# Kernel tuning notes

Hardware: AMD Instinct MI355X
Metric: run time of the kernel (lower is better)

Reference implementation:

```python
import jax, jax.numpy as jnp
import numpy as np
from jax import lax

B, N, M = 2, 16384, 4096
C1, C2 = 128, 256
H1, H2 = 256, 128  # mlp = [C1+C2, 256, 128]


def setup_inputs() -> dict:
    key = jax.random.key(0)
    ks = jax.random.split(key, 8)
    return {
        "unknown": jax.random.normal(ks[0], (B, N, 3), jnp.float32),
        "known": jax.random.normal(ks[1], (B, M, 3), jnp.float32),
        "unknow_feats": jax.random.normal(ks[2], (B, C1, N), jnp.float32),
        "known_feats": jax.random.normal(ks[3], (B, C2, M), jnp.float32),
        "W1": jax.random.normal(ks[4], (H1, C1 + C2), jnp.float32) * 0.05,
        "b1": jnp.zeros((H1,), jnp.float32),
        "W2": jax.random.normal(ks[5], (H2, H1), jnp.float32) * 0.05,
        "b2": jnp.zeros((H2,), jnp.float32),
    }


def reference(unknown, known, unknow_feats, known_feats, W1, b1, W2, b2):
    # Pairwise squared distances (B, n, m) via ||a||^2 + ||b||^2 - 2 a.b
    d2 = (
        jnp.sum(unknown * unknown, -1)[:, :, None]
        + jnp.sum(known * known, -1)[:, None, :]
        - 2.0 * jnp.einsum("bnd,bmd->bnm", unknown, known)
    )
    # 3 nearest neighbors
    neg_d2, idx = lax.top_k(-d2, 3)  # (B, n, 3)
    dist = jnp.sqrt(jnp.maximum(-neg_d2, 0.0))  # pointops returns sqrt distances
    dist_recip = 1.0 / (dist + 1e-8)
    weight = dist_recip / jnp.sum(dist_recip, axis=2, keepdims=True)  # (B, n, 3)
    # Gather neighbor features (B, C2, n, 3) and inverse-distance weighted sum
    gathered = jax.vmap(lambda f, i: f[:, i])(known_feats, idx)
    interpolated = jnp.sum(gathered * weight[:, None, :, :], axis=-1)  # (B, C2, n)
    new_features = jnp.concatenate([interpolated, unknow_feats], axis=1)  # (B, C1+C2, n)
    # Shared MLP (1x1 convs, bn=False -> conv bias + ReLU)
    h = jax.nn.relu(jnp.einsum("oc,bcn->bon", W1, new_features) + b1[None, :, None])
    out = jax.nn.relu(jnp.einsum("oc,bcn->bon", W2, h) + b2[None, :, None])
    return out  # (B, mlp[-1], n)
```

## Files before the change

### kernel.cpp

```cpp
#include <hip/hip_runtime.h>
#include <hip/hip_bf16.h>

#define BB 2
#define NN 16384
#define MM 4096
#define C1 128
#define C2 256
#define CIN 384
#define H1 256
#define H2 128
#define XROW 392
#define HROW 264

typedef __attribute__((ext_vector_type(8))) short bf16x8;
typedef __attribute__((ext_vector_type(4))) float f32x4;
typedef __attribute__((ext_vector_type(2))) float f32x2;

__device__ __forceinline__ short f32_to_bf16(float x) {
    unsigned u = __float_as_uint(x);
    u += 0x7fffu + ((u >> 16) & 1u);
    return (short)(u >> 16);
}
__device__ __forceinline__ float bf16_to_f32(unsigned short u) {
    union { unsigned u; float f; } c; c.u = ((unsigned)u) << 16; return c.f;
}
__device__ __forceinline__ unsigned pack_bf16x2(float a, float b) {
    __hip_bfloat162 h = __float22bfloat162_rn(make_float2(a, b));
    union { __hip_bfloat162 h; unsigned u; } cv;
    cv.h = h;
    return cv.u;
}
__device__ __forceinline__ f32x2 score2l(f32x2 ax2, f32x2 ay2, f32x2 az2,
                                         f32x2 kx, f32x2 ky, f32x2 kz, f32x2 kn) {
    f32x2 t = __builtin_elementwise_fma(ay2, ky, kn);
    t = __builtin_elementwise_fma(ax2, kx, t);
    t = __builtin_elementwise_fma(az2, kz, t);
    return t;
}

__global__ __launch_bounds__(256) void prep_kernel(
    const float* __restrict__ KF, unsigned short* __restrict__ KT16,
    const float* __restrict__ W1, const float* __restrict__ W2,
    short* __restrict__ W1b, short* __restrict__ W2b,
    const float* __restrict__ known, float* __restrict__ kpk8)
{
    const int bx  = blockIdx.x;
    const int tid = threadIdx.x;
    if (bx < 2048) {
        __shared__ float tl[32][33];
        const int b  = bx >> 10;
        const int c0 = ((bx >> 7) & 7) * 32;
        const int m0 = (bx & 127) * 32;
        const int tx = tid & 31;
        const int ty = tid >> 5;
        #pragma unroll
        for (int r = 0; r < 4; ++r) {
            int c = ty + r * 8;
            tl[c][tx] = KF[((size_t)b * C2 + c0 + c) * MM + m0 + tx];
        }
        __syncthreads();
        #pragma unroll
        for (int r = 0; r < 4; ++r) {
            int m = ty + r * 8;
            KT16[((size_t)b * MM + m0 + m) * C2 + c0 + tx] =
                (unsigned short)f32_to_bf16(tl[tx][m]);
        }
    } else if (bx < 2432) {
        int i = (bx - 2048) * 256 + tid;
        if (i < H1 * CIN) W1b[i] = f32_to_bf16(W1[i]);
        if (i < H2 * H1)  W2b[i] = f32_to_bf16(W2[i]);
    } else {
        int i = (bx - 2432) * 256 + tid;
        if (i < BB * MM) {
            float x = known[3 * i + 0], y = known[3 * i + 1], z = known[3 * i + 2];
            float n = fmaf(x, x, fmaf(y, y, z * z));
            int g = i >> 1, j = i & 1;
            float* base = kpk8 + (size_t)g * 8;
            base[0 + j] = x; base[2 + j] = y; base[4 + j] = z; base[6 + j] = n;
        }
    }
}

__global__ __launch_bounds__(1024, 8) void fused_knn_mlp_kernel(
    const float* __restrict__ unknown,
    const float* __restrict__ kpk8,
    const float* __restrict__ unknow_feats,
    const unsigned short* __restrict__ KT16,
    const short* __restrict__ W1b, const float* __restrict__ b1,
    const short* __restrict__ W2b, const float* __restrict__ b2,
    float* __restrict__ out)
{
    __shared__ __align__(16) float cand[16384];
    __shared__ __align__(16) float red[3072];
    __shared__ float vf[64];
    __shared__ int   cnt[64];
    __shared__ int   IsL[64 * 3];
    __shared__ float WsL[64 * 3];

    const int bx    = blockIdx.x;
    const int tid   = threadIdx.x;
    const int lane  = tid & 63;
    const int w     = __builtin_amdgcn_readfirstlane(tid >> 6);
    const int b     = bx >> 8;
    const int qbase = (bx & 255) * 64;
    const int n     = qbase + lane;

    if (tid < 64) cnt[tid] = 0;

    {
        const float* kb = kpk8 + (size_t)b * 16384;
        #pragma unroll
        for (int c = 0; c < 4; ++c) {
            const int i = c * 4096 + tid * 4;
            *(f32x4*)&cand[i] = *(const f32x4*)(kb + i);
        }
    }

    {
        const float ux = unknown[((size_t)b * NN + n) * 3 + 0];
        const float uy = unknown[((size_t)b * NN + n) * 3 + 1];
        const float uz = unknown[((size_t)b * NN + n) * 3 + 2];
        const f32x2 ax2 = {-2.f * ux, -2.f * ux};
        const f32x2 ay2 = {-2.f * uy, -2.f * uy};
        const f32x2 az2 = {-2.f * uz, -2.f * uz};
        const float un = fmaf(ux, ux, fmaf(uy, uy, uz * uz));

        const int gbase = w * 128;
        const float* kw = cand + w * 1024;
        __syncthreads();

        float va0 = 3e38f, va1 = 3e38f, va2 = 3e38f;
        float vb0 = 3e38f, vb1 = 3e38f, vb2 = 3e38f;
        #pragma unroll 4
        for (int g = 0; g < 128; ++g) {
            const f32x4 P = *(const f32x4*)(kw + g * 8);
            const f32x4 Q = *(const f32x4*)(kw + g * 8 + 4);
            const f32x2 kx = {P.x, P.y};
            const f32x2 ky = {P.z, P.w};
            const f32x2 kz = {Q.x, Q.y};
            const f32x2 kn = {Q.z, Q.w};
            const f32x2 sc2 = score2l(ax2, ay2, az2, kx, ky, kz, kn);
            float sa = sc2.x;
            va2 = __builtin_amdgcn_fmed3f(va1, sa, va2);
            va1 = __builtin_amdgcn_fmed3f(va0, sa, va1);
            va0 = fminf(sa, va0);
            float sb = sc2.y;
            vb2 = __builtin_amdgcn_fmed3f(vb1, sb, vb2);
            vb1 = __builtin_amdgcn_fmed3f(vb0, sb, vb1);
            vb0 = fminf(sb, vb0);
        }
        {
            float bv[3] = {vb0, vb1, vb2};
            #pragma unroll
            for (int k = 0; k < 3; ++k) {
                float d = bv[k];
                va2 = __builtin_amdgcn_fmed3f(va1, d, va2);
                va1 = __builtin_amdgcn_fmed3f(va0, d, va1);
                va0 = fminf(d, va0);
            }
        }
        red[(w * 64 + lane) * 3 + 0] = va0;
        red[(w * 64 + lane) * 3 + 1] = va1;
        red[(w * 64 + lane) * 3 + 2] = va2;
        __syncthreads();

        if (tid < 64) {
            float r0 = 3e38f, r1 = 3e38f, r2 = 3e38f;
            #pragma unroll
            for (int ww = 0; ww < 16; ++ww) {
                #pragma unroll
                for (int k = 0; k < 3; ++k) {
                    float d = red[(ww * 64 + tid) * 3 + k];
                    r2 = __builtin_amdgcn_fmed3f(r1, d, r2);
                    r1 = __builtin_amdgcn_fmed3f(r0, d, r1);
                    r0 = fminf(d, r0);
                }
            }
            vf[tid] = r2;
        }
        __syncthreads();

        float* mscp = red;
        int*   midp = (int*)red + 512;
        const float v2f = vf[lane];
        #pragma unroll 4
        for (int g = 0; g < 128; ++g) {
            const f32x4 P = *(const f32x4*)(kw + g * 8);
            const f32x4 Q = *(const f32x4*)(kw + g * 8 + 4);
            const f32x2 kx = {P.x, P.y};
            const f32x2 ky = {P.z, P.w};
            const f32x2 kz = {Q.x, Q.y};
            const f32x2 kn = {Q.z, Q.w};
            const f32x2 sc2 = score2l(ax2, ay2, az2, kx, ky, kz, kn);
            if (fminf(sc2.x, sc2.y) <= v2f) {
                if (sc2.x <= v2f) {
                    int c = atomicAdd(&cnt[lane], 1);
                    if (c < 8) { mscp[lane * 8 + c] = sc2.x; midp[lane * 8 + c] = (gbase + g) * 2; }
                }
                if (sc2.y <= v2f) {
                    int c = atomicAdd(&cnt[lane], 1);
                    if (c < 8) { mscp[lane * 8 + c] = sc2.y; midp[lane * 8 + c] = (gbase + g) * 2 + 1; }
                }
            }
        }
        __syncthreads();

        if (tid < 64) {
            const int c = cnt[tid] < 8 ? cnt[tid] : 8;
            float r0 = 3e38f, r1 = 3e38f, r2 = 3e38f;
            int   q0 = 0x7FFFFFFF, q1 = 0x7FFFFFFF, q2 = 0x7FFFFFFF;
            #pragma unroll
            for (int k = 0; k < 8; ++k) {
                float d = (k < c) ? mscp[tid * 8 + k] : 3e38f;
                int   j = (k < c) ? midp[tid * 8 + k] : 0x7FFFFFFF;
                const bool lt0 = (d < r0) || (d == r0 && j < q0);
                const bool lt1 = (d < r1) || (d == r1 && j < q1);
                const bool lt2 = (d < r2) || (d == r2 && j < q2);
                float nr2 = lt1 ? r1 : (lt2 ? d : r2);
                int   nq2 = lt1 ? q1 : (lt2 ? j : q2);
                float nr1 = lt0 ? r0 : (lt1 ? d : r1);
                int   nq1 = lt0 ? q0 : (lt1 ? j : q1);
                float nr0 = lt0 ? d : r0;
                int   nq0 = lt0 ? j : q0;
                r0 = nr0; r1 = nr1; r2 = nr2; q0 = nq0; q1 = nq1; q2 = nq2;
            }
            float d0 = sqrtf(fmaxf(r0 + un, 0.f));
            float d1 = sqrtf(fmaxf(r1 + un, 0.f));
            float d2 = sqrtf(fmaxf(r2 + un, 0.f));
            float i0 = 1.f / (d0 + 1e-8f);
            float i1 = 1.f / (d1 + 1e-8f);
            float i2 = 1.f / (d2 + 1e-8f);
            float s  = i0 + i1 + i2;
            IsL[tid * 3 + 0] = q0; IsL[tid * 3 + 1] = q1; IsL[tid * 3 + 2] = q2;
            WsL[tid * 3 + 0] = i0 / s; WsL[tid * 3 + 1] = i1 / s; WsL[tid * 3 + 2] = i2 / s;
        }
    }
    __syncthreads();

    const unsigned short* KTb = KT16 + (size_t)b * MM * C2;
    short* XH_s = (short*)cand;
    short* Hs_s = (short*)cand + 32 * XROW;
    const int lr = lane & 15;
    const int lq = lane >> 4;
    const int c4 = lane << 2;

    for (int tile = 0; tile < 2; ++tile) {
        const int pbase = tile * 32;

        {
            ushort4 g[2][3];
            #pragma unroll
            for (int j = 0; j < 2; ++j) {
                const int pi = (pbase + 2 * w + j) * 3;
                g[j][0] = *(const ushort4*)(KTb + (size_t)IsL[pi + 0] * C2 + c4);
                g[j][1] = *(const ushort4*)(KTb + (size_t)IsL[pi + 1] * C2 + c4);
                g[j][2] = *(const ushort4*)(KTb + (size_t)IsL[pi + 2] * C2 + c4);
            }
            #pragma unroll
            for (int j = 0; j < 2; ++j) {
                const int pl = 2 * w + j;
                const int pi = (pbase + pl) * 3;
                const float w0 = WsL[pi + 0], w1 = WsL[pi + 1], w2 = WsL[pi + 2];
                float vx = fmaf(w0, bf16_to_f32(g[j][0].x), fmaf(w1, bf16_to_f32(g[j][1].x), w2 * bf16_to_f32(g[j][2].x)));
                float vy = fmaf(w0, bf16_to_f32(g[j][0].y), fmaf(w1, bf16_to_f32(g[j][1].y), w2 * bf16_to_f32(g[j][2].y)));
                float vz = fmaf(w0, bf16_to_f32(g[j][0].z), fmaf(w1, bf16_to_f32(g[j][1].z), w2 * bf16_to_f32(g[j][2].z)));
                float vw = fmaf(w0, bf16_to_f32(g[j][0].w), fmaf(w1, bf16_to_f32(g[j][1].w), w2 * bf16_to_f32(g[j][2].w)));
                uint2 pk;
                pk.x = pack_bf16x2(vx, vy);
                pk.y = pack_bf16x2(vz, vw);
                *(uint2*)&XH_s[pl * XROW + c4] = pk;
            }
            const float* UFb = unknow_feats + (size_t)b * C1 * NN + qbase + pbase;
            const int cc = tid >> 3;
            const int nq = (tid & 7) << 2;
            const float4 f = *(const float4*)(UFb + (size_t)cc * NN + nq);
            XH_s[(nq + 0) * XROW + C2 + cc] = f32_to_bf16(f.x);
            XH_s[(nq + 1) * XROW + C2 + cc] = f32_to_bf16(f.y);
            XH_s[(nq + 2) * XROW + C2 + cc] = f32_to_bf16(f.z);
            XH_s[(nq + 3) * XROW + C2 + cc] = f32_to_bf16(f.w);
        }
        __syncthreads();

        f32x4 acc1[2];
        acc1[0] = (f32x4){0.f, 0.f, 0.f, 0.f};
        acc1[1] = (f32x4){0.f, 0.f, 0.f, 0.f};
        #pragma unroll 4
        for (int k0 = 0; k0 < CIN; k0 += 32) {
            bf16x8 a  = *(const bf16x8*)(W1b + (size_t)(w * 16 + lr) * CIN + k0 + lq * 8);
            bf16x8 x0 = *(bf16x8*)&XH_s[lr * XROW + k0 + lq * 8];
            bf16x8 x1 = *(bf16x8*)&XH_s[(16 + lr) * XROW + k0 + lq * 8];
            acc1[0] = __builtin_amdgcn_mfma_f32_16x16x32_bf16(a, x0, acc1[0], 0, 0, 0);
            acc1[1] = __builtin_amdgcn_mfma_f32_16x16x32_bf16(a, x1, acc1[1], 0, 0, 0);
        }
        {
            const int ob = w * 16 + lq * 4;
            float bb0 = b1[ob + 0], bb1 = b1[ob + 1], bb2 = b1[ob + 2], bb3 = b1[ob + 3];
            #pragma unroll
            for (int p = 0; p < 2; ++p) {
                uint2 pk;
                pk.x = pack_bf16x2(fmaxf(acc1[p].x + bb0, 0.f),
                                   fmaxf(acc1[p].y + bb1, 0.f));
                pk.y = pack_bf16x2(fmaxf(acc1[p].z + bb2, 0.f),
                                   fmaxf(acc1[p].w + bb3, 0.f));
                *(uint2*)&Hs_s[(p * 16 + lr) * HROW + ob] = pk;
            }
        }
        __syncthreads();

        {
            const int r0 = (w & 7) * 16;
            const int pg = (w >> 3) * 16;
            f32x4 acc2 = (f32x4){0.f, 0.f, 0.f, 0.f};
            #pragma unroll 4
            for (int k0 = 0; k0 < H1; k0 += 32) {
                bf16x8 a2 = *(const bf16x8*)(W2b + (size_t)(r0 + lr) * H1 + k0 + lq * 8);
                bf16x8 h  = *(bf16x8*)&Hs_s[(pg + lr) * HROW + k0 + lq * 8];
                acc2 = __builtin_amdgcn_mfma_f32_16x16x32_bf16(a2, h, acc2, 0, 0, 0);
            }
            const int nn = qbase + pbase + pg + lr;
            #pragma unroll
            for (int r = 0; r < 4; ++r) {
                const int o = r0 + lq * 4 + r;
                out[((size_t)b * H2 + o) * NN + nn] =
                    fmaxf(((const float*)&acc2)[r] + b2[o], 0.f);
            }
        }
        __syncthreads();
    }
}

extern "C" void kernel_launch(void* const* d_in, const int* in_sizes, int n_in,
                              void* d_out, int out_size, void* d_ws, size_t ws_size,
                              hipStream_t stream) {
    const float* unknown      = (const float*)d_in[0];
    const float* known        = (const float*)d_in[1];
    const float* unknow_feats = (const float*)d_in[2];
    const float* known_feats  = (const float*)d_in[3];
    const float* W1           = (const float*)d_in[4];
    const float* b1           = (const float*)d_in[5];
    const float* W2           = (const float*)d_in[6];
    const float* b2           = (const float*)d_in[7];
    float* out = (float*)d_out;

    char* ws = (char*)d_ws;
    short*          W1b  = (short*)(ws);
    short*          W2b  = (short*)(ws + 196608);
    float*          kpk8 = (float*)(ws + 262144);
    unsigned short* KT16 = (unsigned short*)(ws + 393216);

    prep_kernel<<<2464, 256, 0, stream>>>(
        known_feats, KT16, W1, W2, W1b, W2b, known, kpk8);

    fused_knn_mlp_kernel<<<512, 1024, 0, stream>>>(
        unknown, kpk8, unknow_feats, KT16, W1b, b1, W2b, b2, out);
}
```

Measured before the change: 158.8 us.

## Process two query sets per thread to reuse shared-memory candidate loads

Each block now handles 128 queries instead of 64. Each thread scores two queries against every known point it reads from LDS, so the cost of loading the shared candidate set is spread over twice as many queries. The grid is halved to 256 blocks, and the reduction and candidate buffers and the MLP tile loop grow to match. In exchange it raises register pressure and leaves only 256 blocks, which may not fill the GPU, with more serial MLP work per block.

```diff
diff --git a/kernel.cpp b/kernel.cpp
--- a/kernel.cpp
+++ b/kernel.cpp
@@ -81,7 +81,7 @@
     }
 }
 
-__global__ __launch_bounds__(1024, 8) void fused_knn_mlp_kernel(
+__global__ __launch_bounds__(1024, 4) void fused_knn_mlp_kernel(
     const float* __restrict__ unknown,
     const float* __restrict__ kpk8,
     const float* __restrict__ unknow_feats,
@@ -91,21 +91,20 @@
     float* __restrict__ out)
 {
     __shared__ __align__(16) float cand[16384];
-    __shared__ __align__(16) float red[3072];
-    __shared__ float vf[64];
-    __shared__ int   cnt[64];
-    __shared__ int   IsL[64 * 3];
-    __shared__ float WsL[64 * 3];
+    __shared__ __align__(16) float red[6144];
+    __shared__ float vf[128];
+    __shared__ int   cnt[128];
+    __shared__ int   IsL[128 * 3];
+    __shared__ float WsL[128 * 3];
 
     const int bx    = blockIdx.x;
     const int tid   = threadIdx.x;
     const int lane  = tid & 63;
     const int w     = __builtin_amdgcn_readfirstlane(tid >> 6);
-    const int b     = bx >> 8;
-    const int qbase = (bx & 255) * 64;
-    const int n     = qbase + lane;
-
-    if (tid < 64) cnt[tid] = 0;
+    const int b     = bx >> 7;
+    const int qbase = (bx & 127) * 128;
+
+    if (tid < 128) cnt[tid] = 0;
 
     {
         const float* kb = kpk8 + (size_t)b * 16384;
@@ -117,13 +116,16 @@
     }
 
     {
-        const float ux = unknown[((size_t)b * NN + n) * 3 + 0];
-        const float uy = unknown[((size_t)b * NN + n) * 3 + 1];
-        const float uz = unknown[((size_t)b * NN + n) * 3 + 2];
-        const f32x2 ax2 = {-2.f * ux, -2.f * ux};
-        const f32x2 ay2 = {-2.f * uy, -2.f * uy};
-        const f32x2 az2 = {-2.f * uz, -2.f * uz};
-        const float un = fmaf(ux, ux, fmaf(uy, uy, uz * uz));
+        const float* u0 = unknown + ((size_t)b * NN + qbase + lane) * 3;
+        const float* u1 = unknown + ((size_t)b * NN + qbase + 64 + lane) * 3;
+        const float ux0 = u0[0], uy0 = u0[1], uz0 = u0[2];
+        const float ux1 = u1[0], uy1 = u1[1], uz1 = u1[2];
+        const f32x2 ax0 = {-2.f * ux0, -2.f * ux0};
+        const f32x2 ay0 = {-2.f * uy0, -2.f * uy0};
+        const f32x2 az0 = {-2.f * uz0, -2.f * uz0};
+        const f32x2 ax1 = {-2.f * ux1, -2.f * ux1};
+        const f32x2 ay1 = {-2.f * uy1, -2.f * uy1};
+        const f32x2 az1 = {-2.f * uz1, -2.f * uz1};
 
         const int gbase = w * 128;
         const float* kw = cand + w * 1024;
@@ -131,6 +133,8 @@
 
         float va0 = 3e38f, va1 = 3e38f, va2 = 3e38f;
         float vb0 = 3e38f, vb1 = 3e38f, vb2 = 3e38f;
+        float wa0 = 3e38f, wa1 = 3e38f, wa2 = 3e38f;
+        float wb0 = 3e38f, wb1 = 3e38f, wb2 = 3e38f;
         #pragma unroll 4
         for (int g = 0; g < 128; ++g) {
             const f32x4 P = *(const f32x4*)(kw + g * 8);
@@ -139,15 +143,28 @@
             const f32x2 ky = {P.z, P.w};
             const f32x2 kz = {Q.x, Q.y};
             const f32x2 kn = {Q.z, Q.w};
-            const f32x2 sc2 = score2l(ax2, ay2, az2, kx, ky, kz, kn);
-            float sa = sc2.x;
-            va2 = __builtin_amdgcn_fmed3f(va1, sa, va2);
-            va1 = __builtin_amdgcn_fmed3f(va0, sa, va1);
-            va0 = fminf(sa, va0);
-            float sb = sc2.y;
-            vb2 = __builtin_amdgcn_fmed3f(vb1, sb, vb2);
-            vb1 = __builtin_amdgcn_fmed3f(vb0, sb, vb1);
-            vb0 = fminf(sb, vb0);
+            const f32x2 s0 = score2l(ax0, ay0, az0, kx, ky, kz, kn);
+            const f32x2 s1 = score2l(ax1, ay1, az1, kx, ky, kz, kn);
+            {
+                float sa = s0.x;
+                va2 = __builtin_amdgcn_fmed3f(va1, sa, va2);
+                va1 = __builtin_amdgcn_fmed3f(va0, sa, va1);
+                va0 = fminf(sa, va0);
+                float sb = s0.y;
+                vb2 = __builtin_amdgcn_fmed3f(vb1, sb, vb2);
+                vb1 = __builtin_amdgcn_fmed3f(vb0, sb, vb1);
+                vb0 = fminf(sb, vb0);
+            }
+            {
+                float sa = s1.x;
+                wa2 = __builtin_amdgcn_fmed3f(wa1, sa, wa2);
+                wa1 = __builtin_amdgcn_fmed3f(wa0, sa, wa1);
+                wa0 = fminf(sa, wa0);
+                float sb = s1.y;
+                wb2 = __builtin_amdgcn_fmed3f(wb1, sb, wb2);
+                wb1 = __builtin_amdgcn_fmed3f(wb0, sb, wb1);
+                wb0 = fminf(sb, wb0);
+            }
         }
         {
             float bv[3] = {vb0, vb1, vb2};
@@ -158,19 +175,30 @@
                 va1 = __builtin_amdgcn_fmed3f(va0, d, va1);
                 va0 = fminf(d, va0);
             }
-        }
-        red[(w * 64 + lane) * 3 + 0] = va0;
-        red[(w * 64 + lane) * 3 + 1] = va1;
-        red[(w * 64 + lane) * 3 + 2] = va2;
-        __syncthreads();
-
-        if (tid < 64) {
+            float cv[3] = {wb0, wb1, wb2};
+            #pragma unroll
+            for (int k = 0; k < 3; ++k) {
+                float d = cv[k];
+                wa2 = __builtin_amdgcn_fmed3f(wa1, d, wa2);
+                wa1 = __builtin_amdgcn_fmed3f(wa0, d, wa1);
+                wa0 = fminf(d, wa0);
+            }
+        }
+        red[(w * 128 + lane) * 3 + 0] = va0;
+        red[(w * 128 + lane) * 3 + 1] = va1;
+        red[(w * 128 + lane) * 3 + 2] = va2;
+        red[(w * 128 + 64 + lane) * 3 + 0] = wa0;
+        red[(w * 128 + 64 + lane) * 3 + 1] = wa1;
+        red[(w * 128 + 64 + lane) * 3 + 2] = wa2;
+        __syncthreads();
+
+        if (tid < 128) {
             float r0 = 3e38f, r1 = 3e38f, r2 = 3e38f;
             #pragma unroll
             for (int ww = 0; ww < 16; ++ww) {
                 #pragma unroll
                 for (int k = 0; k < 3; ++k) {
-                    float d = red[(ww * 64 + tid) * 3 + k];
+                    float d = red[(ww * 128 + tid) * 3 + k];
                     r2 = __builtin_amdgcn_fmed3f(r1, d, r2);
                     r1 = __builtin_amdgcn_fmed3f(r0, d, r1);
                     r0 = fminf(d, r0);
@@ -181,8 +209,9 @@
         __syncthreads();
 
         float* mscp = red;
-        int*   midp = (int*)red + 512;
-        const float v2f = vf[lane];
+        int*   midp = (int*)red + 1024;
+        const float v2f0 = vf[lane];
+        const float v2f1 = vf[64 + lane];
         #pragma unroll 4
         for (int g = 0; g < 128; ++g) {
             const f32x4 P = *(const f32x4*)(kw + g * 8);
@@ -191,21 +220,32 @@
             const f32x2 ky = {P.z, P.w};
             const f32x2 kz = {Q.x, Q.y};
             const f32x2 kn = {Q.z, Q.w};
-            const f32x2 sc2 = score2l(ax2, ay2, az2, kx, ky, kz, kn);
-            if (fminf(sc2.x, sc2.y) <= v2f) {
-                if (sc2.x <= v2f) {
+            const f32x2 s0 = score2l(ax0, ay0, az0, kx, ky, kz, kn);
+            const f32x2 s1 = score2l(ax1, ay1, az1, kx, ky, kz, kn);
+            const bool h0 = fminf(s0.x, s0.y) <= v2f0;
+            const bool h1 = fminf(s1.x, s1.y) <= v2f1;
+            if (h0 || h1) {
+                if (s0.x <= v2f0) {
                     int c = atomicAdd(&cnt[lane], 1);
-                    if (c < 8) { mscp[lane * 8 + c] = sc2.x; midp[lane * 8 + c] = (gbase + g) * 2; }
-                }
-                if (sc2.y <= v2f) {
+                    if (c < 8) { mscp[lane * 8 + c] = s0.x; midp[lane * 8 + c] = (gbase + g) * 2; }
+                }
+                if (s0.y <= v2f0) {
                     int c = atomicAdd(&cnt[lane], 1);
-                    if (c < 8) { mscp[lane * 8 + c] = sc2.y; midp[lane * 8 + c] = (gbase + g) * 2 + 1; }
-                }
-            }
-        }
-        __syncthreads();
-
-        if (tid < 64) {
+                    if (c < 8) { mscp[lane * 8 + c] = s0.y; midp[lane * 8 + c] = (gbase + g) * 2 + 1; }
+                }
+                if (s1.x <= v2f1) {
+                    int c = atomicAdd(&cnt[64 + lane], 1);
+                    if (c < 8) { mscp[(64 + lane) * 8 + c] = s1.x; midp[(64 + lane) * 8 + c] = (gbase + g) * 2; }
+                }
+                if (s1.y <= v2f1) {
+                    int c = atomicAdd(&cnt[64 + lane], 1);
+                    if (c < 8) { mscp[(64 + lane) * 8 + c] = s1.y; midp[(64 + lane) * 8 + c] = (gbase + g) * 2 + 1; }
+                }
+            }
+        }
+        __syncthreads();
+
+        if (tid < 128) {
             const int c = cnt[tid] < 8 ? cnt[tid] : 8;
             float r0 = 3e38f, r1 = 3e38f, r2 = 3e38f;
             int   q0 = 0x7FFFFFFF, q1 = 0x7FFFFFFF, q2 = 0x7FFFFFFF;
@@ -224,6 +264,9 @@
                 int   nq0 = lt0 ? j : q0;
                 r0 = nr0; r1 = nr1; r2 = nr2; q0 = nq0; q1 = nq1; q2 = nq2;
             }
+            const float* up = unknown + ((size_t)b * NN + qbase + tid) * 3;
+            const float uxx = up[0], uyy = up[1], uzz = up[2];
+            const float un = fmaf(uxx, uxx, fmaf(uyy, uyy, uzz * uzz));
             float d0 = sqrtf(fmaxf(r0 + un, 0.f));
             float d1 = sqrtf(fmaxf(r1 + un, 0.f));
             float d2 = sqrtf(fmaxf(r2 + un, 0.f));
@@ -244,7 +287,7 @@
     const int lq = lane >> 4;
     const int c4 = lane << 2;
 
-    for (int tile = 0; tile < 2; ++tile) {
+    for (int tile = 0; tile < 4; ++tile) {
         const int pbase = tile * 32;
 
         {
@@ -351,6 +394,6 @@
     prep_kernel<<<2464, 256, 0, stream>>>(
         known_feats, KT16, W1, W2, W1b, W2b, known, kpk8);
 
-    fused_knn_mlp_kernel<<<512, 1024, 0, stream>>>(
+    fused_knn_mlp_kernel<<<256, 1024, 0, stream>>>(
         unknown, kpk8, unknow_feats, KT16, W1b, b1, W2b, b2, out);
 }
```

Result: slower. 170.6 us (+7.4%).

## Split KNN candidate reads between LDS and global memory across waves

Applied to the files above, without the earlier changes.

Only the even-wave slices of the known-point candidates are staged into LDS, while odd waves read their candidates straight from global memory (L1/L2) using 32-byte vector loads. The goal is to halve the LDS fill traffic and spread load bandwidth across the LDS and vector-memory paths. It adds a second score variant with a different FMA order for odd waves, which could change tie behaviour slightly, and odd waves now depend on cache latency. It also recomputes the query norm in the final selection step from global memory.

```diff
diff --git a/kernel.cpp b/kernel.cpp
--- a/kernel.cpp
+++ b/kernel.cpp
@@ -15,6 +15,7 @@
 typedef __attribute__((ext_vector_type(8))) short bf16x8;
 typedef __attribute__((ext_vector_type(4))) float f32x4;
 typedef __attribute__((ext_vector_type(2))) float f32x2;
+typedef __attribute__((ext_vector_type(8))) float f32x8;
 
 __device__ __forceinline__ short f32_to_bf16(float x) {
     unsigned u = __float_as_uint(x);
@@ -36,6 +37,13 @@
     t = __builtin_elementwise_fma(ax2, kx, t);
     t = __builtin_elementwise_fma(az2, kz, t);
     return t;
+}
+__device__ __forceinline__ f32x2 score2s(f32x2 ax2, f32x2 ay2, f32x2 az2,
+                                         f32x2 kx, f32x2 ky, f32x2 kz, f32x2 kn) {
+    f32x2 t = ay2 * ky;
+    t = __builtin_elementwise_fma(ax2, kx, t);
+    t = __builtin_elementwise_fma(az2, kz, t);
+    return t + kn;
 }
 
 __global__ __launch_bounds__(256) void prep_kernel(
@@ -110,9 +118,12 @@
     {
         const float* kb = kpk8 + (size_t)b * 16384;
         #pragma unroll
-        for (int c = 0; c < 4; ++c) {
+        for (int c = 0; c < 2; ++c) {
             const int i = c * 4096 + tid * 4;
-            *(f32x4*)&cand[i] = *(const f32x4*)(kb + i);
+            const int slot = i >> 10;
+            const int off  = i & 1023;
+            const int a    = (slot * 2) * 1024 + off;
+            *(f32x4*)&cand[a] = *(const f32x4*)(kb + a);
         }
     }
 
@@ -127,27 +138,48 @@
 
         const int gbase = w * 128;
         const float* kw = cand + w * 1024;
+        const float* kg = kpk8 + ((size_t)b * 2048 + gbase) * 8;
         __syncthreads();
 
         float va0 = 3e38f, va1 = 3e38f, va2 = 3e38f;
         float vb0 = 3e38f, vb1 = 3e38f, vb2 = 3e38f;
-        #pragma unroll 4
-        for (int g = 0; g < 128; ++g) {
-            const f32x4 P = *(const f32x4*)(kw + g * 8);
-            const f32x4 Q = *(const f32x4*)(kw + g * 8 + 4);
-            const f32x2 kx = {P.x, P.y};
-            const f32x2 ky = {P.z, P.w};
-            const f32x2 kz = {Q.x, Q.y};
-            const f32x2 kn = {Q.z, Q.w};
-            const f32x2 sc2 = score2l(ax2, ay2, az2, kx, ky, kz, kn);
-            float sa = sc2.x;
-            va2 = __builtin_amdgcn_fmed3f(va1, sa, va2);
-            va1 = __builtin_amdgcn_fmed3f(va0, sa, va1);
-            va0 = fminf(sa, va0);
-            float sb = sc2.y;
-            vb2 = __builtin_amdgcn_fmed3f(vb1, sb, vb2);
-            vb1 = __builtin_amdgcn_fmed3f(vb0, sb, vb1);
-            vb0 = fminf(sb, vb0);
+        if ((w & 1) == 0) {
+            #pragma unroll 4
+            for (int g = 0; g < 128; ++g) {
+                const f32x4 P = *(const f32x4*)(kw + g * 8);
+                const f32x4 Q = *(const f32x4*)(kw + g * 8 + 4);
+                const f32x2 kx = {P.x, P.y};
+                const f32x2 ky = {P.z, P.w};
+                const f32x2 kz = {Q.x, Q.y};
+                const f32x2 kn = {Q.z, Q.w};
+                const f32x2 sc2 = score2l(ax2, ay2, az2, kx, ky, kz, kn);
+                float sa = sc2.x;
+                va2 = __builtin_amdgcn_fmed3f(va1, sa, va2);
+                va1 = __builtin_amdgcn_fmed3f(va0, sa, va1);
+                va0 = fminf(sa, va0);
+                float sb = sc2.y;
+                vb2 = __builtin_amdgcn_fmed3f(vb1, sb, vb2);
+                vb1 = __builtin_amdgcn_fmed3f(vb0, sb, vb1);
+                vb0 = fminf(sb, vb0);
+            }
+        } else {
+            #pragma unroll 4
+            for (int g = 0; g < 128; ++g) {
+                const f32x8 G = *(const f32x8*)(kg + (size_t)g * 8);
+                const f32x2 kx = __builtin_shufflevector(G, G, 0, 1);
+                const f32x2 ky = __builtin_shufflevector(G, G, 2, 3);
+                const f32x2 kz = __builtin_shufflevector(G, G, 4, 5);
+                const f32x2 kn = __builtin_shufflevector(G, G, 6, 7);
+                const f32x2 sc2 = score2s(ax2, ay2, az2, kx, ky, kz, kn);
+                float sa = sc2.x;
+                va2 = __builtin_amdgcn_fmed3f(va1, sa, va2);
+                va1 = __builtin_amdgcn_fmed3f(va0, sa, va1);
+                va0 = fminf(sa, va0);
+                float sb = sc2.y;
+                vb2 = __builtin_amdgcn_fmed3f(vb1, sb, vb2);
+                vb1 = __builtin_amdgcn_fmed3f(vb0, sb, vb1);
+                vb0 = fminf(sb, vb0);
+            }
         }
         {
             float bv[3] = {vb0, vb1, vb2};
@@ -183,23 +215,45 @@
         float* mscp = red;
         int*   midp = (int*)red + 512;
         const float v2f = vf[lane];
-        #pragma unroll 4
-        for (int g = 0; g < 128; ++g) {
-            const f32x4 P = *(const f32x4*)(kw + g * 8);
-            const f32x4 Q = *(const f32x4*)(kw + g * 8 + 4);
-            const f32x2 kx = {P.x, P.y};
-            const f32x2 ky = {P.z, P.w};
-            const f32x2 kz = {Q.x, Q.y};
-            const f32x2 kn = {Q.z, Q.w};
-            const f32x2 sc2 = score2l(ax2, ay2, az2, kx, ky, kz, kn);
-            if (fminf(sc2.x, sc2.y) <= v2f) {
-                if (sc2.x <= v2f) {
-                    int c = atomicAdd(&cnt[lane], 1);
-                    if (c < 8) { mscp[lane * 8 + c] = sc2.x; midp[lane * 8 + c] = (gbase + g) * 2; }
+        if ((w & 1) == 0) {
+            #pragma unroll 4
+            for (int g = 0; g < 128; ++g) {
+                const f32x4 P = *(const f32x4*)(kw + g * 8);
+                const f32x4 Q = *(const f32x4*)(kw + g * 8 + 4);
+                const f32x2 kx = {P.x, P.y};
+                const f32x2 ky = {P.z, P.w};
+                const f32x2 kz = {Q.x, Q.y};
+                const f32x2 kn = {Q.z, Q.w};
+                const f32x2 sc2 = score2l(ax2, ay2, az2, kx, ky, kz, kn);
+                if (fminf(sc2.x, sc2.y) <= v2f) {
+                    if (sc2.x <= v2f) {
+                        int c = atomicAdd(&cnt[lane], 1);
+                        if (c < 8) { mscp[lane * 8 + c] = sc2.x; midp[lane * 8 + c] = (gbase + g) * 2; }
+                    }
+                    if (sc2.y <= v2f) {
+                        int c = atomicAdd(&cnt[lane], 1);
+                        if (c < 8) { mscp[lane * 8 + c] = sc2.y; midp[lane * 8 + c] = (gbase + g) * 2 + 1; }
+                    }
                 }
-                if (sc2.y <= v2f) {
-                    int c = atomicAdd(&cnt[lane], 1);
-                    if (c < 8) { mscp[lane * 8 + c] = sc2.y; midp[lane * 8 + c] = (gbase + g) * 2 + 1; }
+            }
+        } else {
+            #pragma unroll 4
+            for (int g = 0; g < 128; ++g) {
+                const f32x8 G = *(const f32x8*)(kg + (size_t)g * 8);
+                const f32x2 kx = __builtin_shufflevector(G, G, 0, 1);
+                const f32x2 ky = __builtin_shufflevector(G, G, 2, 3);
+                const f32x2 kz = __builtin_shufflevector(G, G, 4, 5);
+                const f32x2 kn = __builtin_shufflevector(G, G, 6, 7);
+                const f32x2 sc2 = score2s(ax2, ay2, az2, kx, ky, kz, kn);
+                if (fminf(sc2.x, sc2.y) <= v2f) {
+                    if (sc2.x <= v2f) {
+                        int c = atomicAdd(&cnt[lane], 1);
+                        if (c < 8) { mscp[lane * 8 + c] = sc2.x; midp[lane * 8 + c] = (gbase + g) * 2; }
+                    }
+                    if (sc2.y <= v2f) {
+                        int c = atomicAdd(&cnt[lane], 1);
+                        if (c < 8) { mscp[lane * 8 + c] = sc2.y; midp[lane * 8 + c] = (gbase + g) * 2 + 1; }
+                    }
                 }
             }
         }
@@ -224,9 +278,12 @@
                 int   nq0 = lt0 ? j : q0;
                 r0 = nr0; r1 = nr1; r2 = nr2; q0 = nq0; q1 = nq1; q2 = nq2;
             }
-            float d0 = sqrtf(fmaxf(r0 + un, 0.f));
-            float d1 = sqrtf(fmaxf(r1 + un, 0.f));
-            float d2 = sqrtf(fmaxf(r2 + un, 0.f));
+            const float* up = unknown + ((size_t)b * NN + qbase + tid) * 3;
+            const float uxx = up[0], uyy = up[1], uzz = up[2];
+            const float unq = fmaf(uxx, uxx, fmaf(uyy, uyy, uzz * uzz));
+            float d0 = sqrtf(fmaxf(r0 + unq, 0.f));
+            float d1 = sqrtf(fmaxf(r1 + unq, 0.f));
+            float d2 = sqrtf(fmaxf(r2 + unq, 0.f));
             float i0 = 1.f / (d0 + 1e-8f);
             float i1 = 1.f / (d1 + 1e-8f);
             float i2 = 1.f / (d2 + 1e-8f);
```

New measurement: 163.3 us. +2.9%, slower.
